# Kernel tuning notes

Hardware: AMD Instinct MI355X
Metric: run time of the kernel (lower is better)

Reference implementation:

```python
import jax, jax.numpy as jnp
import numpy as np

B, S, E, H = 2, 2048, 1024, 16
D = E // H  # head dim = 64


def setup_inputs() -> dict:
    key = jax.random.key(0)
    ks = jax.random.split(key, 9)
    sc = 0.02
    return {
        "inputs": jax.random.normal(ks[0], (B, S, E), jnp.float32),
        "Wq": jax.random.normal(ks[1], (E, E), jnp.float32) * sc,
        "bq": jnp.zeros((E,), jnp.float32),
        "Wk": jax.random.normal(ks[2], (E, E), jnp.float32) * sc,
        "bk": jnp.zeros((E,), jnp.float32),
        "Wv": jax.random.normal(ks[3], (E, E), jnp.float32) * sc,
        "bv": jnp.zeros((E,), jnp.float32),
        "Wo": jax.random.normal(ks[4], (E, E), jnp.float32) * sc,
        "bo": jnp.zeros((E,), jnp.float32),
    }


def _split_heads(x):
    # [B, S, E] -> [B, H, S, D]
    b, s, _ = x.shape
    return x.reshape(b, s, H, D).transpose(0, 2, 1, 3)


def reference(inputs, Wq, bq, Wk, bk, Wv, bv, Wo, bo):
    q = _split_heads(inputs @ Wq + bq)
    k = _split_heads(inputs @ Wk + bk)
    v = _split_heads(inputs @ Wv + bv)

    # scaled dot-product scores: [B, H, S, S]
    score = jnp.einsum("bhqd,bhkd->bhqk", q, k) / jnp.sqrt(jnp.float32(D))

    # causal mask, exactly as the original: score*mask - 10000*(1-mask)
    i = jnp.arange(S)[:, None]
    j = jnp.arange(S)[None, :]
    mask = (i >= j).astype(score.dtype)  # square case of i >= j - S + S
    score = score * mask - 10000.0 * (1.0 - mask)

    weights = jax.nn.softmax(score, axis=-1)
    attn = jnp.einsum("bhqk,bhkd->bhqd", weights, v)  # [B, H, S, D]
    attn = attn.transpose(0, 2, 1, 3).reshape(inputs.shape[0], S, E)
    return attn @ Wo + bo
```

## Files before the change

kernel.cpp:

```cpp
#include <hip/hip_runtime.h>
#include <stdint.h>

#define Bc 2
#define Sc 2048
#define Ec 1024
#define Hc 16
#define Dc 64
#define Mc (Bc*Sc)

typedef __attribute__((ext_vector_type(4))) float f32x4;
typedef __attribute__((ext_vector_type(8))) short bf16x8v;

#define SCL 0.1803368801f

__device__ __forceinline__ unsigned short f2bf(float f){
  unsigned int u = __float_as_uint(f);
  u += 0x7FFFu + ((u >> 16) & 1u);
  return (unsigned short)(u >> 16);
}

__global__ __launch_bounds__(256) void k_prep(const float* __restrict__ X,
                                              unsigned short* __restrict__ Xb,
                                              const float* __restrict__ W0, const float* __restrict__ W1,
                                              const float* __restrict__ W2, const float* __restrict__ W3,
                                              unsigned short* __restrict__ WT4){
  __shared__ float st[64][65];
  int bx = blockIdx.x, t = threadIdx.x;
  if (bx < 4096){
    int i = bx*256 + t;
    float4 v = ((const float4*)X)[i];
    ushort4 o;
    o.x = f2bf(v.x); o.y = f2bf(v.y); o.z = f2bf(v.z); o.w = f2bf(v.w);
    ((ushort4*)Xb)[i] = o;
  } else {
    int id = bx - 4096;
    int z = id >> 8, rem = id & 255;
    int k0 = (rem >> 4)*64, n0 = (rem & 15)*64;
    const float* W = (z==0)?W0 : (z==1)?W1 : (z==2)?W2 : W3;
    unsigned short* o = WT4 + (size_t)z * Ec * Ec;
    #pragma unroll
    for (int i=0;i<16;i++){ int lin=i*256+t; int r=lin>>6, c=lin&63;
      st[r][c] = W[(size_t)(k0+r)*Ec + n0+c]; }
    __syncthreads();
    #pragma unroll
    for (int i=0;i<16;i++){ int lin=i*256+t; int nn=lin>>6, kk=lin&63;
      o[(size_t)(n0+nn)*Ec + k0+kk] = f2bf(st[kk][nn]); }
  }
}

__global__ __launch_bounds__(256,2) void k_qkv(const unsigned short* __restrict__ A,
                                               const unsigned short* __restrict__ WT4,
                                               const float* __restrict__ bq,
                                               const float* __restrict__ bk,
                                               const float* __restrict__ bv,
                                               unsigned short* __restrict__ QKV){
  __shared__ unsigned short sA[2][128*32];
  __shared__ unsigned short sB[2][3][64*32];
  int bm = blockIdx.y, bn = blockIdx.x;
  int t = threadIdx.x, w = t>>6, lane = t&63, quad = lane>>4, m16 = lane&15;
  int wm = w>>1, wn = w&1;
  f32x4 acc[3][4][2];
  #pragma unroll
  for (int z=0;z<3;z++)
    #pragma unroll
    for (int i=0;i<4;i++)
      #pragma unroll
      for (int j=0;j<2;j++) acc[z][i][j] = (f32x4){0.f,0.f,0.f,0.f};

  auto stage = [&](int kt, int buf){
    #pragma unroll
    for (int i=0;i<2;i++){
      int cb = (w*2 + i)*64;
      int L = cb + lane;
      int row = L>>2, c = (L&3)*8;
      const unsigned short* ga = A + (size_t)(bm*128 + row)*Ec + kt*32 + c;
      __builtin_amdgcn_global_load_lds((const __attribute__((address_space(1))) void*)ga,
          (__attribute__((address_space(3))) void*)(&sA[buf][0] + cb*8), 16, 0, 0);
    }
    #pragma unroll
    for (int z=0;z<3;z++){
      int cb = w*64;
      int L = cb + lane;
      int row = L>>2, c = (L&3)*8;
      const unsigned short* gb = WT4 + (size_t)z*Ec*Ec + (size_t)(bn*64 + row)*Ec + kt*32 + c;
      __builtin_amdgcn_global_load_lds((const __attribute__((address_space(1))) void*)gb,
          (__attribute__((address_space(3))) void*)(&sB[buf][z][0] + cb*8), 16, 0, 0);
    }
  };

  stage(0, 0);
  for (int kt=0; kt<Ec/32; ++kt){
    int cur = kt & 1;
    __syncthreads();
    if (kt+1 < Ec/32) stage(kt+1, cur^1);
    bf16x8v af[4];
    #pragma unroll
    for (int s=0;s<4;s++)
      af[s] = *(const bf16x8v*)(&sA[cur][0] + (wm*64 + s*16 + m16)*32 + quad*8);
    #pragma unroll
    for (int z=0;z<3;z++){
      bf16x8v bfr[2];
      #pragma unroll
      for (int s=0;s<2;s++)
        bfr[s] = *(const bf16x8v*)(&sB[cur][z][0] + (wn*32 + s*16 + m16)*32 + quad*8);
      #pragma unroll
      for (int sm=0;sm<4;sm++)
        #pragma unroll
        for (int sn=0;sn<2;sn++)
          acc[z][sm][sn] = __builtin_amdgcn_mfma_f32_16x16x32_bf16(af[sm], bfr[sn], acc[z][sm][sn], 0,0,0);
    }
  }
  #pragma unroll
  for (int z=0;z<3;z++){
    const float* bias = (z==0)?bq : (z==1)?bk : bv;
    unsigned short* Out = QKV + (size_t)z * (size_t)Mc * Ec;
    #pragma unroll
    for (int sm=0;sm<4;sm++){
      int row0 = bm*128 + wm*64 + sm*16 + quad*4;
      int bidx = row0 >> 11;
      #pragma unroll
      for (int sn=0;sn<2;sn++){
        int col = bn*64 + wn*32 + sn*16 + m16;
        float bb = bias[col];
        int h = col >> 6, d = col & 63;
        if (z == 2){
          int s0 = row0 & (Sc-1);
          ushort4 pk;
          pk.x = f2bf(acc[z][sm][sn][0] + bb);
          pk.y = f2bf(acc[z][sm][sn][1] + bb);
          pk.z = f2bf(acc[z][sm][sn][2] + bb);
          pk.w = f2bf(acc[z][sm][sn][3] + bb);
          *(ushort4*)(Out + (((size_t)bidx*Hc + h)*Dc + d)*Sc + s0) = pk;
        } else {
          float sc_ = (z==0) ? SCL : 1.0f;
          #pragma unroll
          for (int r=0;r<4;r++){
            int s = (row0 + r) & (Sc-1);
            Out[(((size_t)bidx*Hc + h)*Sc + s)*Dc + d] = f2bf((acc[z][sm][sn][r] + bb)*sc_);
          }
        }
      }
    }
  }
}

__global__ __launch_bounds__(256,4) void k_gemm1(const unsigned short* __restrict__ A,
                                                 const unsigned short* __restrict__ WT,
                                                 const float* __restrict__ bias,
                                                 float* __restrict__ Out){
  __shared__ unsigned short sA[2][128*32];
  __shared__ unsigned short sB[2][64*32];
  int bm = blockIdx.y, bn = blockIdx.x;
  int t = threadIdx.x, w = t>>6, lane = t&63, quad = lane>>4, m16 = lane&15;
  int wm = w>>1, wn = w&1;
  f32x4 acc[4][2];
  #pragma unroll
  for (int i=0;i<4;i++)
    #pragma unroll
    for (int j=0;j<2;j++) acc[i][j] = (f32x4){0.f,0.f,0.f,0.f};

  auto stage = [&](int kt, int buf){
    #pragma unroll
    for (int i=0;i<2;i++){
      int cb = (w*2 + i)*64;
      int L = cb + lane;
      int row = L>>2, c = (L&3)*8;
      const unsigned short* ga = A + (size_t)(bm*128 + row)*Ec + kt*32 + c;
      __builtin_amdgcn_global_load_lds((const __attribute__((address_space(1))) void*)ga,
          (__attribute__((address_space(3))) void*)(&sA[buf][0] + cb*8), 16, 0, 0);
    }
    {
      int cb = w*64;
      int L = cb + lane;
      int row = L>>2, c = (L&3)*8;
      const unsigned short* gb = WT + (size_t)(bn*64 + row)*Ec + kt*32 + c;
      __builtin_amdgcn_global_load_lds((const __attribute__((address_space(1))) void*)gb,
          (__attribute__((address_space(3))) void*)(&sB[buf][0] + cb*8), 16, 0, 0);
    }
  };

  stage(0, 0);
  for (int kt=0; kt<Ec/32; ++kt){
    int cur = kt & 1;
    __syncthreads();
    if (kt+1 < Ec/32) stage(kt+1, cur^1);
    bf16x8v af[4], bfr[2];
    #pragma unroll
    for (int s=0;s<4;s++)
      af[s]  = *(const bf16x8v*)(&sA[cur][0] + (wm*64 + s*16 + m16)*32 + quad*8);
    #pragma unroll
    for (int s=0;s<2;s++)
      bfr[s] = *(const bf16x8v*)(&sB[cur][0] + (wn*32 + s*16 + m16)*32 + quad*8);
    #pragma unroll
    for (int sm=0;sm<4;sm++)
      #pragma unroll
      for (int sn=0;sn<2;sn++)
        acc[sm][sn] = __builtin_amdgcn_mfma_f32_16x16x32_bf16(af[sm], bfr[sn], acc[sm][sn], 0,0,0);
  }
  #pragma unroll
  for (int sm=0;sm<4;sm++){
    int row0 = bm*128 + wm*64 + sm*16 + quad*4;
    #pragma unroll
    for (int sn=0;sn<2;sn++){
      int col = bn*64 + wn*32 + sn*16 + m16;
      float bb = bias[col];
      #pragma unroll
      for (int r=0;r<4;r++)
        Out[(size_t)(row0+r)*Ec + col] = acc[sm][sn][r] + bb;
    }
  }
}

__device__ __forceinline__ void attn_tile(const unsigned short* sK, const unsigned short* sVT,
                                          unsigned short* pw, bf16x8v qf0, bf16x8v qf1,
                                          bf16x8v ones, f32x4& li, f32x4* Oa,
                                          int kbase, int qw, int quad, int m16){
  int sw = m16 & 7;
  f32x4 sc[4];
  #pragma unroll
  for (int sm=0;sm<4;sm++){
    int row = sm*16 + m16;
    bf16x8v kf0 = *(const bf16x8v*)(sK + row*64 + ((quad  )^sw)*8);
    bf16x8v kf1 = *(const bf16x8v*)(sK + row*64 + ((quad+4)^sw)*8);
    f32x4 a = (f32x4){0.f,0.f,0.f,0.f};
    a = __builtin_amdgcn_mfma_f32_16x16x32_bf16(kf0, qf0, a, 0,0,0);
    a = __builtin_amdgcn_mfma_f32_16x16x32_bf16(kf1, qf1, a, 0,0,0);
    sc[sm] = a;
  }
  if (kbase + 63 > qw){
    #pragma unroll
    for (int sm=0;sm<4;sm++)
      #pragma unroll
      for (int r=0;r<4;r++){
        int kg = kbase + sm*16 + quad*4 + r;
        float p = exp2f(sc[sm][r]);
        sc[sm][r] = (kg <= qw + m16) ? p : 0.0f;
      }
  } else {
    #pragma unroll
    for (int sm=0;sm<4;sm++)
      #pragma unroll
      for (int r=0;r<4;r++) sc[sm][r] = exp2f(sc[sm][r]);
  }

  #pragma unroll
  for (int sm=0;sm<4;sm++){
    ushort4 pk;
    pk.x = f2bf(sc[sm][0]); pk.y = f2bf(sc[sm][1]);
    pk.z = f2bf(sc[sm][2]); pk.w = f2bf(sc[sm][3]);
    int chunk = sm*2 + (quad>>1);
    *(ushort4*)(pw + m16*64 + (chunk^sw)*8 + (quad&1)*4) = pk;
  }
  bf16x8v pf0 = *(const bf16x8v*)(pw + m16*64 + ((quad  )^sw)*8);
  bf16x8v pf1 = *(const bf16x8v*)(pw + m16*64 + ((quad+4)^sw)*8);

  li = __builtin_amdgcn_mfma_f32_16x16x32_bf16(pf0, ones, li, 0,0,0);
  li = __builtin_amdgcn_mfma_f32_16x16x32_bf16(pf1, ones, li, 0,0,0);

  #pragma unroll
  for (int tt=0;tt<4;tt++){
    int rowv = tt*16 + m16;
    bf16x8v vf0 = *(const bf16x8v*)(sVT + rowv*64 + ((quad  )^sw)*8);
    bf16x8v vf1 = *(const bf16x8v*)(sVT + rowv*64 + ((quad+4)^sw)*8);
    Oa[tt] = __builtin_amdgcn_mfma_f32_16x16x32_bf16(pf0, vf0, Oa[tt], 0,0,0);
    Oa[tt] = __builtin_amdgcn_mfma_f32_16x16x32_bf16(pf1, vf1, Oa[tt], 0,0,0);
  }
}

__global__ __launch_bounds__(256,2) void k_attn(const unsigned short* __restrict__ Qb,
                                                const unsigned short* __restrict__ Kb,
                                                const unsigned short* __restrict__ VTb,
                                                unsigned short* __restrict__ Ob){
  __shared__ unsigned short sK [64*64];
  __shared__ unsigned short sVT[64*64];
  __shared__ unsigned short sP [4][16*64];
  int bh = blockIdx.y;
  int qtA = (int)blockIdx.x;
  int qtB = 31 - qtA;
  size_t base = (size_t)bh * Sc * Dc;
  const unsigned short* Q  = Qb  + base;
  const unsigned short* K  = Kb  + base;
  const unsigned short* VT = VTb + base;
  int t = threadIdx.x, w = t>>6, lane = t&63, quad = lane>>4, m16 = lane&15;
  int qwA = qtA*64 + w*16;
  int qwB = qtB*64 + w*16;

  bf16x8v qA0 = *(const bf16x8v*)(Q + (size_t)(qwA + m16)*Dc + quad*8);
  bf16x8v qA1 = *(const bf16x8v*)(Q + (size_t)(qwA + m16)*Dc + 32 + quad*8);
  bf16x8v qB0 = *(const bf16x8v*)(Q + (size_t)(qwB + m16)*Dc + quad*8);
  bf16x8v qB1 = *(const bf16x8v*)(Q + (size_t)(qwB + m16)*Dc + 32 + quad*8);

  bf16x8v ones;
  #pragma unroll
  for (int i=0;i<8;i++) ones[i] = (short)0x3F80;

  f32x4 OaA[4], OaB[4];
  #pragma unroll
  for (int i=0;i<4;i++){ OaA[i] = (f32x4){0.f,0.f,0.f,0.f}; OaB[i] = (f32x4){0.f,0.f,0.f,0.f}; }
  f32x4 liA = (f32x4){0.f,0.f,0.f,0.f}, liB = (f32x4){0.f,0.f,0.f,0.f};

  unsigned short* pw = &sP[w][0];

  for (int kt=0; kt<=qtB; ++kt){
    int kbase = kt*64;
    #pragma unroll
    for (int i=0;i<2;i++){
      int cb = (w*2 + i)*64;
      int L = cb + lane;
      int row = L>>3, p = L&7, c = p ^ (row&7);
      const unsigned short* gk = K  + (size_t)(kbase+row)*Dc + c*8;
      const unsigned short* gv = VT + (size_t)row*Sc + kbase + c*8;
      __builtin_amdgcn_global_load_lds((const __attribute__((address_space(1))) void*)gk,
          (__attribute__((address_space(3))) void*)(sK + cb*8), 16, 0, 0);
      __builtin_amdgcn_global_load_lds((const __attribute__((address_space(1))) void*)gv,
          (__attribute__((address_space(3))) void*)(sVT + cb*8), 16, 0, 0);
    }
    __syncthreads();

    if (kt <= qtA)
      attn_tile(sK, sVT, pw, qA0, qA1, ones, liA, OaA, kbase, qwA, quad, m16);
    attn_tile(sK, sVT, pw, qB0, qB1, ones, liB, OaB, kbase, qwB, quad, m16);

    __syncthreads();
  }

  int b = bh >> 4, h = bh & 15;
  float iA[4], iB[4];
  #pragma unroll
  for (int r=0;r<4;r++){ iA[r] = 1.0f/liA[r]; iB[r] = 1.0f/liB[r]; }
  #pragma unroll
  for (int tt=0;tt<4;tt++)
    #pragma unroll
    for (int r=0;r<4;r++){
      int e = h*64 + tt*16 + m16;
      int sA_ = qwA + quad*4 + r;
      int sB_ = qwB + quad*4 + r;
      Ob[((size_t)b*Sc + sA_)*Ec + e] = f2bf(OaA[tt][r]*iA[r]);
      Ob[((size_t)b*Sc + sB_)*Ec + e] = f2bf(OaB[tt][r]*iB[r]);
    }
}

extern "C" void kernel_launch(void* const* d_in, const int* in_sizes, int n_in,
                              void* d_out, int out_size, void* d_ws, size_t ws_size,
                              hipStream_t stream){
  const float* X  = (const float*)d_in[0];
  const float* Wq = (const float*)d_in[1];
  const float* bq = (const float*)d_in[2];
  const float* Wk = (const float*)d_in[3];
  const float* bk = (const float*)d_in[4];
  const float* Wv = (const float*)d_in[5];
  const float* bv = (const float*)d_in[6];
  const float* Wo = (const float*)d_in[7];
  const float* bo = (const float*)d_in[8];

  uint8_t* ws = (uint8_t*)d_ws;
  unsigned short* Xb  = (unsigned short*)(ws);
  unsigned short* WT4 = (unsigned short*)(ws + (size_t)(8u<<20));
  unsigned short* QKV = (unsigned short*)(ws + (size_t)(16u<<20));
  unsigned short* ATT = (unsigned short*)(ws + (size_t)(40u<<20));

  k_prep<<<dim3(5120), 256, 0, stream>>>(X, Xb, Wq, Wk, Wv, Wo, WT4);
  k_qkv<<<dim3(16,32), 256, 0, stream>>>(Xb, WT4, bq, bk, bv, QKV);
  k_attn<<<dim3(16,32), 256, 0, stream>>>(QKV, QKV + (size_t)Mc*Ec, QKV + 2*(size_t)Mc*Ec, ATT);
  k_gemm1<<<dim3(16,32), 256, 0, stream>>>(ATT, WT4 + (size_t)3*Ec*Ec, bo, (float*)d_out);
}
```

Before: 208.2 us.

## Double GEMM K-tile to 64 with XOR-swizzled LDS, batch two KV tiles per attention sync

The QKV and output-projection GEMMs now stage 64-wide K tiles instead of 32, using an XOR swizzle on the LDS column index to avoid bank conflicts. This halves the number of barrier-separated iterations and doubles the MFMA work per sync. The output GEMM's launch bound drops from 4 to 2 blocks per CU to make room for the larger LDS footprint. The attention kernel loads two K/V tiles per barrier pair into two buffers and processes both before syncing, which halves the syncs but gives no overlap between load and compute.

```diff
diff --git a/kernel.cpp b/kernel.cpp
--- a/kernel.cpp
+++ b/kernel.cpp
@@ -18,6 +18,10 @@
   u += 0x7FFFu + ((u >> 16) & 1u);
   return (unsigned short)(u >> 16);
 }
+
+#define GLDS(src, dst) __builtin_amdgcn_global_load_lds( \
+    (const __attribute__((address_space(1))) void*)(src), \
+    (__attribute__((address_space(3))) void*)(dst), 16, 0, 0)
 
 __global__ __launch_bounds__(256) void k_prep(const float* __restrict__ X,
                                               unsigned short* __restrict__ Xb,
@@ -54,11 +58,11 @@
                                                const float* __restrict__ bk,
                                                const float* __restrict__ bv,
                                                unsigned short* __restrict__ QKV){
-  __shared__ unsigned short sA[2][128*32];
-  __shared__ unsigned short sB[2][3][64*32];
+  __shared__ unsigned short sA[2][128*64];
+  __shared__ unsigned short sB[2][3][64*64];
   int bm = blockIdx.y, bn = blockIdx.x;
   int t = threadIdx.x, w = t>>6, lane = t&63, quad = lane>>4, m16 = lane&15;
-  int wm = w>>1, wn = w&1;
+  int wm = w>>1, wn = w&1, sw = m16 & 7;
   f32x4 acc[3][4][2];
   #pragma unroll
   for (int z=0;z<3;z++)
@@ -69,45 +73,52 @@
 
   auto stage = [&](int kt, int buf){
     #pragma unroll
-    for (int i=0;i<2;i++){
-      int cb = (w*2 + i)*64;
+    for (int i=0;i<4;i++){
+      int cb = (w*4 + i)*64;
       int L = cb + lane;
-      int row = L>>2, c = (L&3)*8;
-      const unsigned short* ga = A + (size_t)(bm*128 + row)*Ec + kt*32 + c;
-      __builtin_amdgcn_global_load_lds((const __attribute__((address_space(1))) void*)ga,
-          (__attribute__((address_space(3))) void*)(&sA[buf][0] + cb*8), 16, 0, 0);
+      int row = L>>3, c = (L&7) ^ (row&7);
+      GLDS(A + (size_t)(bm*128 + row)*Ec + kt*64 + c*8, &sA[buf][0] + cb*8);
+    }
+    #pragma unroll
+    for (int z=0;z<3;z++)
+      #pragma unroll
+      for (int i=0;i<2;i++){
+        int cb = (w*2 + i)*64;
+        int L = cb + lane;
+        int row = L>>3, c = (L&7) ^ (row&7);
+        GLDS(WT4 + (size_t)z*Ec*Ec + (size_t)(bn*64 + row)*Ec + kt*64 + c*8,
+             &sB[buf][z][0] + cb*8);
+      }
+  };
+
+  stage(0, 0);
+  for (int kt=0; kt<Ec/64; ++kt){
+    int cur = kt & 1;
+    __syncthreads();
+    if (kt+1 < Ec/64) stage(kt+1, cur^1);
+    bf16x8v af[4][2];
+    #pragma unroll
+    for (int s=0;s<4;s++){
+      int row = wm*64 + s*16 + m16;
+      af[s][0] = *(const bf16x8v*)(&sA[cur][0] + row*64 + ((quad  )^sw)*8);
+      af[s][1] = *(const bf16x8v*)(&sA[cur][0] + row*64 + ((quad+4)^sw)*8);
     }
     #pragma unroll
     for (int z=0;z<3;z++){
-      int cb = w*64;
-      int L = cb + lane;
-      int row = L>>2, c = (L&3)*8;
-      const unsigned short* gb = WT4 + (size_t)z*Ec*Ec + (size_t)(bn*64 + row)*Ec + kt*32 + c;
-      __builtin_amdgcn_global_load_lds((const __attribute__((address_space(1))) void*)gb,
-          (__attribute__((address_space(3))) void*)(&sB[buf][z][0] + cb*8), 16, 0, 0);
-    }
-  };
-
-  stage(0, 0);
-  for (int kt=0; kt<Ec/32; ++kt){
-    int cur = kt & 1;
-    __syncthreads();
-    if (kt+1 < Ec/32) stage(kt+1, cur^1);
-    bf16x8v af[4];
-    #pragma unroll
-    for (int s=0;s<4;s++)
-      af[s] = *(const bf16x8v*)(&sA[cur][0] + (wm*64 + s*16 + m16)*32 + quad*8);
-    #pragma unroll
-    for (int z=0;z<3;z++){
-      bf16x8v bfr[2];
-      #pragma unroll
-      for (int s=0;s<2;s++)
-        bfr[s] = *(const bf16x8v*)(&sB[cur][z][0] + (wn*32 + s*16 + m16)*32 + quad*8);
+      bf16x8v bfr[2][2];
+      #pragma unroll
+      for (int sn=0;sn<2;sn++){
+        int rowb = wn*32 + sn*16 + m16;
+        bfr[sn][0] = *(const bf16x8v*)(&sB[cur][z][0] + rowb*64 + ((quad  )^sw)*8);
+        bfr[sn][1] = *(const bf16x8v*)(&sB[cur][z][0] + rowb*64 + ((quad+4)^sw)*8);
+      }
       #pragma unroll
       for (int sm=0;sm<4;sm++)
         #pragma unroll
-        for (int sn=0;sn<2;sn++)
-          acc[z][sm][sn] = __builtin_amdgcn_mfma_f32_16x16x32_bf16(af[sm], bfr[sn], acc[z][sm][sn], 0,0,0);
+        for (int sn=0;sn<2;sn++){
+          acc[z][sm][sn] = __builtin_amdgcn_mfma_f32_16x16x32_bf16(af[sm][0], bfr[sn][0], acc[z][sm][sn], 0,0,0);
+          acc[z][sm][sn] = __builtin_amdgcn_mfma_f32_16x16x32_bf16(af[sm][1], bfr[sn][1], acc[z][sm][sn], 0,0,0);
+        }
     }
   }
   #pragma unroll
@@ -144,15 +155,15 @@
   }
 }
 
-__global__ __launch_bounds__(256,4) void k_gemm1(const unsigned short* __restrict__ A,
+__global__ __launch_bounds__(256,2) void k_gemm1(const unsigned short* __restrict__ A,
                                                  const unsigned short* __restrict__ WT,
                                                  const float* __restrict__ bias,
                                                  float* __restrict__ Out){
-  __shared__ unsigned short sA[2][128*32];
-  __shared__ unsigned short sB[2][64*32];
+  __shared__ unsigned short sA[2][128*64];
+  __shared__ unsigned short sB[2][64*64];
   int bm = blockIdx.y, bn = blockIdx.x;
   int t = threadIdx.x, w = t>>6, lane = t&63, quad = lane>>4, m16 = lane&15;
-  int wm = w>>1, wn = w&1;
+  int wm = w>>1, wn = w&1, sw = m16 & 7;
   f32x4 acc[4][2];
   #pragma unroll
   for (int i=0;i<4;i++)
@@ -160,42 +171,47 @@
     for (int j=0;j<2;j++) acc[i][j] = (f32x4){0.f,0.f,0.f,0.f};
 
   auto stage = [&](int kt, int buf){
+    #pragma unroll
+    for (int i=0;i<4;i++){
+      int cb = (w*4 + i)*64;
+      int L = cb + lane;
+      int row = L>>3, c = (L&7) ^ (row&7);
+      GLDS(A + (size_t)(bm*128 + row)*Ec + kt*64 + c*8, &sA[buf][0] + cb*8);
+    }
     #pragma unroll
     for (int i=0;i<2;i++){
       int cb = (w*2 + i)*64;
       int L = cb + lane;
-      int row = L>>2, c = (L&3)*8;
-      const unsigned short* ga = A + (size_t)(bm*128 + row)*Ec + kt*32 + c;
-      __builtin_amdgcn_global_load_lds((const __attribute__((address_space(1))) void*)ga,
-          (__attribute__((address_space(3))) void*)(&sA[buf][0] + cb*8), 16, 0, 0);
-    }
-    {
-      int cb = w*64;
-      int L = cb + lane;
-      int row = L>>2, c = (L&3)*8;
-      const unsigned short* gb = WT + (size_t)(bn*64 + row)*Ec + kt*32 + c;
-      __builtin_amdgcn_global_load_lds((const __attribute__((address_space(1))) void*)gb,
-          (__attribute__((address_space(3))) void*)(&sB[buf][0] + cb*8), 16, 0, 0);
+      int row = L>>3, c = (L&7) ^ (row&7);
+      GLDS(WT + (size_t)(bn*64 + row)*Ec + kt*64 + c*8, &sB[buf][0] + cb*8);
     }
   };
 
   stage(0, 0);
-  for (int kt=0; kt<Ec/32; ++kt){
+  for (int kt=0; kt<Ec/64; ++kt){
     int cur = kt & 1;
     __syncthreads();
-    if (kt+1 < Ec/32) stage(kt+1, cur^1);
-    bf16x8v af[4], bfr[2];
-    #pragma unroll
-    for (int s=0;s<4;s++)
-      af[s]  = *(const bf16x8v*)(&sA[cur][0] + (wm*64 + s*16 + m16)*32 + quad*8);
-    #pragma unroll
-    for (int s=0;s<2;s++)
-      bfr[s] = *(const bf16x8v*)(&sB[cur][0] + (wn*32 + s*16 + m16)*32 + quad*8);
+    if (kt+1 < Ec/64) stage(kt+1, cur^1);
+    bf16x8v af[4][2], bfr[2][2];
+    #pragma unroll
+    for (int s=0;s<4;s++){
+      int row = wm*64 + s*16 + m16;
+      af[s][0] = *(const bf16x8v*)(&sA[cur][0] + row*64 + ((quad  )^sw)*8);
+      af[s][1] = *(const bf16x8v*)(&sA[cur][0] + row*64 + ((quad+4)^sw)*8);
+    }
+    #pragma unroll
+    for (int sn=0;sn<2;sn++){
+      int rowb = wn*32 + sn*16 + m16;
+      bfr[sn][0] = *(const bf16x8v*)(&sB[cur][0] + rowb*64 + ((quad  )^sw)*8);
+      bfr[sn][1] = *(const bf16x8v*)(&sB[cur][0] + rowb*64 + ((quad+4)^sw)*8);
+    }
     #pragma unroll
     for (int sm=0;sm<4;sm++)
       #pragma unroll
-      for (int sn=0;sn<2;sn++)
-        acc[sm][sn] = __builtin_amdgcn_mfma_f32_16x16x32_bf16(af[sm], bfr[sn], acc[sm][sn], 0,0,0);
+      for (int sn=0;sn<2;sn++){
+        acc[sm][sn] = __builtin_amdgcn_mfma_f32_16x16x32_bf16(af[sm][0], bfr[sn][0], acc[sm][sn], 0,0,0);
+        acc[sm][sn] = __builtin_amdgcn_mfma_f32_16x16x32_bf16(af[sm][1], bfr[sn][1], acc[sm][sn], 0,0,0);
+      }
   }
   #pragma unroll
   for (int sm=0;sm<4;sm++){
@@ -271,8 +287,8 @@
                                                 const unsigned short* __restrict__ Kb,
                                                 const unsigned short* __restrict__ VTb,
                                                 unsigned short* __restrict__ Ob){
-  __shared__ unsigned short sK [64*64];
-  __shared__ unsigned short sVT[64*64];
+  __shared__ unsigned short sK [2][64*64];
+  __shared__ unsigned short sVT[2][64*64];
   __shared__ unsigned short sP [4][16*64];
   int bh = blockIdx.y;
   int qtA = (int)blockIdx.x;
@@ -301,26 +317,32 @@
 
   unsigned short* pw = &sP[w][0];
 
-  for (int kt=0; kt<=qtB; ++kt){
+  auto stage = [&](int kt, int buf){
     int kbase = kt*64;
     #pragma unroll
     for (int i=0;i<2;i++){
       int cb = (w*2 + i)*64;
       int L = cb + lane;
       int row = L>>3, p = L&7, c = p ^ (row&7);
-      const unsigned short* gk = K  + (size_t)(kbase+row)*Dc + c*8;
-      const unsigned short* gv = VT + (size_t)row*Sc + kbase + c*8;
-      __builtin_amdgcn_global_load_lds((const __attribute__((address_space(1))) void*)gk,
-          (__attribute__((address_space(3))) void*)(sK + cb*8), 16, 0, 0);
-      __builtin_amdgcn_global_load_lds((const __attribute__((address_space(1))) void*)gv,
-          (__attribute__((address_space(3))) void*)(sVT + cb*8), 16, 0, 0);
-    }
+      GLDS(K  + (size_t)(kbase+row)*Dc + c*8,        &sK[buf][0]  + cb*8);
+      GLDS(VT + (size_t)row*Sc + kbase + c*8,        &sVT[buf][0] + cb*8);
+    }
+  };
+
+  for (int kt=0; kt<=qtB; kt+=2){
+    stage(kt, 0);
+    bool have2 = (kt+1 <= qtB);
+    if (have2) stage(kt+1, 1);
     __syncthreads();
 
     if (kt <= qtA)
-      attn_tile(sK, sVT, pw, qA0, qA1, ones, liA, OaA, kbase, qwA, quad, m16);
-    attn_tile(sK, sVT, pw, qB0, qB1, ones, liB, OaB, kbase, qwB, quad, m16);
-
+      attn_tile(&sK[0][0], &sVT[0][0], pw, qA0, qA1, ones, liA, OaA, kt*64, qwA, quad, m16);
+    attn_tile(&sK[0][0], &sVT[0][0], pw, qB0, qB1, ones, liB, OaB, kt*64, qwB, quad, m16);
+    if (have2){
+      if (kt+1 <= qtA)
+        attn_tile(&sK[1][0], &sVT[1][0], pw, qA0, qA1, ones, liA, OaA, (kt+1)*64, qwA, quad, m16);
+      attn_tile(&sK[1][0], &sVT[1][0], pw, qB0, qB1, ones, liB, OaB, (kt+1)*64, qwB, quad, m16);
+    }
     __syncthreads();
   }
 
```

Result: faster. 182.4 us (-12.4%).
